# Kernel optimization log

Measured on AMD Instinct MI355X. Metric: run time of the kernel, lower is better.

Reference implementation:

```python
import jax, jax.numpy as jnp
import numpy as np

N = 8192      # nodes
E = 16384     # edges
G = 512       # graphs
IN = 235      # node feature dim (input_dim)
H = 64        # hidden_dim
ED = 52       # edge feature dim


def setup_inputs() -> dict:
    key = jax.random.key(0)
    ks = jax.random.split(key, 24)
    s = lambda fan_in: 1.0 / np.sqrt(fan_in)
    inp = {}
    inp["x"] = jax.random.normal(ks[0], (N, IN), dtype=jnp.float32)
    inp["edge_index"] = jax.random.randint(ks[1], (2, E), 0, N)
    inp["edge_attr"] = jax.random.uniform(ks[2], (E, ED), dtype=jnp.float32)
    inp["batch"] = jnp.sort(jax.random.randint(ks[3], (N,), 0, G))
    # EdgeModel (nn of nnconv1): Linear(52,128) -> Linear(128, 235*64)
    inp["W1"] = jax.random.normal(ks[4], (128, ED), dtype=jnp.float32) * s(ED)
    inp["b1"] = jnp.zeros((128,), jnp.float32)
    inp["W2"] = jax.random.normal(ks[5], (IN * H, 128), dtype=jnp.float32) * s(128)
    inp["b2"] = jnp.zeros((IN * H,), jnp.float32)
    # NNConv root weight and bias
    inp["root"] = jax.random.normal(ks[6], (IN, H), dtype=jnp.float32) * s(IN)
    inp["conv_b"] = jnp.zeros((H,), jnp.float32)
    # MLP head
    inp["fw1"] = jax.random.normal(ks[7], (128, H), dtype=jnp.float32) * s(H)
    inp["fb1"] = jnp.zeros((128,), jnp.float32)
    inp["fw2"] = jax.random.normal(ks[8], (256, 128), dtype=jnp.float32) * s(128)
    inp["fb2"] = jnp.zeros((256,), jnp.float32)
    inp["fw3"] = jax.random.normal(ks[9], (128, 256), dtype=jnp.float32) * s(256)
    inp["fb3"] = jnp.zeros((128,), jnp.float32)
    inp["fw4"] = jax.random.normal(ks[10], (1, 128), dtype=jnp.float32) * s(128)
    inp["fb4"] = jnp.zeros((1,), jnp.float32)
    return inp


def reference(x, edge_index, edge_attr, batch, W1, b1, W2, b2, root, conv_b,
              fw1, fb1, fw2, fb2, fw3, fb3, fw4, fb4):
    src, dst = edge_index[0], edge_index[1]
    # edge MLP -> per-edge weight matrices [E, IN, H]
    h = edge_attr @ W1.T + b1
    w = (h @ W2.T + b2).reshape(E, IN, H)
    # gather source node feats, per-edge matmul, scatter-add to destinations
    msg = jnp.einsum('ei,eih->eh', x[src], w)          # [E, H]
    agg = jax.ops.segment_sum(msg, dst, num_segments=N)  # [N, H]
    out = jax.nn.relu(agg + x @ root + conv_b)           # NNConv + ReLU
    # global mean pool per graph
    summ = jax.ops.segment_sum(out, batch, num_segments=G)
    cnt = jax.ops.segment_sum(jnp.ones((N, 1), out.dtype), batch, num_segments=G)
    pooled = summ / jnp.maximum(cnt, 1.0)                # [G, H]
    # dense MLP head
    y = jax.nn.relu(pooled @ fw1.T + fb1)
    y = jax.nn.relu(y @ fw2.T + fb2)
    y = jax.nn.relu(y @ fw3.T + fb3)
    return y @ fw4.T + fb4                               # [G, 1]
```

## Files before the change

### kernel.cpp

```cpp
#include <hip/hip_runtime.h>
#include <hip/hip_bf16.h>
#include <stdint.h>

#define N_NODES 8192
#define N_EDGES 16384
#define N_GRAPHS 512
#define IN_DIM 235
#define H_DIM 64
#define ED_DIM 52
#define HID1 128
#define KP 256
#define NB 3328
#define NBE 3456
#define NBP 3584

typedef __bf16 bf16x8 __attribute__((ext_vector_type(8)));
typedef float f32x4 __attribute__((ext_vector_type(4)));

static __device__ inline unsigned short f2bf(float f) {
    union { float f; unsigned u; } v; v.f = f;
    unsigned r = v.u + 0x7FFFu + ((v.u >> 16) & 1u);
    return (unsigned short)(r >> 16);
}
static __device__ inline float bf2f(unsigned short s) {
    union { unsigned u; float f; } v; v.u = ((unsigned)s) << 16;
    return v.f;
}

__global__ __launch_bounds__(256) void k_build_bt(const float* __restrict__ W1,
                                                  const float* __restrict__ W2,
                                                  unsigned short* __restrict__ Bt) {
    __shared__ float w1s[13 * HID1];
    __shared__ float w2s[64 * 132];
    const int i = blockIdx.x;
    const int by = blockIdx.y;
    const int t = threadIdx.x;
    const int dbase = by * 13;
    for (int j = t; j < 13 * HID1; j += 256) {
        const int dd = j >> 7, k = j & 127;
        w1s[j] = W1[k * ED_DIM + dbase + dd];
    }
    const float* w2src = W2 + (size_t)i * 64 * HID1;
    for (int j = t; j < 64 * HID1; j += 256) w2s[(j >> 7) * 132 + (j & 127)] = w2src[j];
    __syncthreads();
    const int pend = by * 832 + 832;
    for (int p = by * 832 + t; p < pend; p += 256) {
        const int dd = (p >> 6) - dbase, h = p & 63;
        const float4* w1v = (const float4*)&w1s[dd * HID1];
        const float4* w2v = (const float4*)&w2s[h * 132];
        float acc = 0.f;
        #pragma unroll
        for (int k4 = 0; k4 < HID1 / 4; ++k4) {
            const float4 a = w1v[k4], b = w2v[k4];
            acc += a.x * b.x + a.y * b.y + a.z * b.z + a.w * b.w;
        }
        Bt[(size_t)p * KP + i] = f2bf(acc);
    }
}

__global__ __launch_bounds__(256) void k_build_ext(const float* __restrict__ root,
                                                   const float* __restrict__ W2,
                                                   const float* __restrict__ b1,
                                                   const float* __restrict__ b2,
                                                   unsigned short* __restrict__ Bt) {
    const int j = blockIdx.x;
    const int i = threadIdx.x;
    if (i >= IN_DIM) return;
    float v;
    if (j < 64) {
        v = root[i * H_DIM + j];
    } else {
        const int jj = i * H_DIM + (j - 64);
        float acc = b2[jj];
        const float* w = W2 + (size_t)jj * HID1;
        #pragma unroll 8
        for (int k = 0; k < HID1; ++k) acc += w[k] * b1[k];
        v = acc;
    }
    Bt[(size_t)(NB + j) * KP + i] = f2bf(v);
}

__global__ __launch_bounds__(256) void k_build_a(const float* __restrict__ x,
                                                 unsigned short* __restrict__ A) {
    const int j = blockIdx.x * 256 + threadIdx.x;
    const int n = j >> 8, i = j & 255;
    A[j] = (i < IN_DIM) ? f2bf(x[n * IN_DIM + i]) : (unsigned short)0;
}

__global__ __launch_bounds__(512, 2) void k_gemm(const unsigned short* __restrict__ A,
                                                 const unsigned short* __restrict__ Bt,
                                                 unsigned short* __restrict__ P,
                                                 float* __restrict__ agg,
                                                 float* __restrict__ xb2,
                                                 const float* __restrict__ conv_b) {
    __shared__ unsigned short As[2 * 256 * 32];
    __shared__ unsigned short Bs[2 * 256 * 32];
    const int t = threadIdx.x;
    const int m0 = blockIdx.y * 256, n0 = blockIdx.x * 256;
    const int wid = t >> 6, lane = t & 63;
    const int wm = wid & 1;
    const int wn = wid >> 1;
    const int q = lane >> 4, r16 = lane & 15;

    f32x4 acc[8][4] = {};

    auto stage = [&](int k0, int buf) {
        #pragma unroll
        for (int r = 0; r < 2; ++r) {
            const int idx = r * 512 + t;
            const int row = idx >> 2;
            const int lgrp = ((idx & 3) ^ ((row >> 1) & 3)) * 8;
            const unsigned short* ga = &A[(size_t)(m0 + row) * KP + k0 + lgrp];
            const unsigned short* gb = &Bt[(size_t)(n0 + row) * KP + k0 + lgrp];
            char* la = (char*)As + buf * 16384 + r * 8192 + wid * 1024;
            char* lb = (char*)Bs + buf * 16384 + r * 8192 + wid * 1024;
            __builtin_amdgcn_global_load_lds(
                (const __attribute__((address_space(1))) unsigned int*)ga,
                (__attribute__((address_space(3))) unsigned int*)la, 16, 0, 0);
            __builtin_amdgcn_global_load_lds(
                (const __attribute__((address_space(1))) unsigned int*)gb,
                (__attribute__((address_space(3))) unsigned int*)lb, 16, 0, 0);
        }
    };

    stage(0, 0);
    const int pcq = (q ^ ((r16 >> 1) & 3)) * 8;
    #pragma unroll
    for (int it = 0; it < 8; ++it) {
        __syncthreads();
        if (it < 7) stage((it + 1) * 32, (it + 1) & 1);
        const int bo = (it & 1) * 8192;
        bf16x8 af[8], bfr[4];
        #pragma unroll
        for (int mi = 0; mi < 8; ++mi)
            af[mi] = *(const bf16x8*)(&As[bo + (wm * 128 + mi * 16 + r16) * 32 + pcq]);
        #pragma unroll
        for (int ni = 0; ni < 4; ++ni)
            bfr[ni] = *(const bf16x8*)(&Bs[bo + (wn * 64 + ni * 16 + r16) * 32 + pcq]);
        #pragma unroll
        for (int mi = 0; mi < 8; ++mi)
            #pragma unroll
            for (int ni = 0; ni < 4; ++ni)
                acc[mi][ni] = __builtin_amdgcn_mfma_f32_16x16x32_bf16(
                    bfr[ni], af[mi], acc[mi][ni], 0, 0, 0);
    }

    if (n0 < NB) {
        #pragma unroll
        for (int mi = 0; mi < 8; ++mi)
            #pragma unroll
            for (int ni = 0; ni < 4; ++ni) {
                const int row = m0 + wm * 128 + mi * 16 + r16;
                const int col = n0 + wn * 64 + ni * 16 + q * 4;
                union { unsigned short us[4]; uint2 u2; } pk;
                #pragma unroll
                for (int rr = 0; rr < 4; ++rr) pk.us[rr] = f2bf(acc[mi][ni][rr]);
                *(uint2*)(&P[(size_t)row * NB + col]) = pk.u2;
            }
    } else if (wn < 2) {
        #pragma unroll
        for (int mi = 0; mi < 8; ++mi)
            #pragma unroll
            for (int ni = 0; ni < 4; ++ni) {
                const int row = m0 + wm * 128 + mi * 16 + r16;
                const int cl = ni * 16 + q * 4;
                if (wn == 0) {
                    const float4 cb = *(const float4*)&conv_b[cl];
                    float4 v;
                    v.x = acc[mi][ni][0] + cb.x; v.y = acc[mi][ni][1] + cb.y;
                    v.z = acc[mi][ni][2] + cb.z; v.w = acc[mi][ni][3] + cb.w;
                    *(float4*)(&agg[row * H_DIM + cl]) = v;
                } else {
                    float4 v;
                    v.x = acc[mi][ni][0]; v.y = acc[mi][ni][1];
                    v.z = acc[mi][ni][2]; v.w = acc[mi][ni][3];
                    *(float4*)(&xb2[row * H_DIM + cl]) = v;
                }
            }
    }
}

__global__ __launch_bounds__(256) void k_edge(const int* __restrict__ ei,
                                              const float* __restrict__ ea,
                                              const unsigned short* __restrict__ P,
                                              const float* __restrict__ xb2,
                                              float* __restrict__ agg) {
    const int e = (blockIdx.x * 256 + threadIdx.x) >> 6;
    const int h = threadIdx.x & 63;
    if (e >= N_EDGES) return;
    const int s = ei[e], dst = ei[N_EDGES + e];
    const unsigned short* Pr = P + (size_t)s * NB + h;
    const float* ear = ea + (size_t)e * ED_DIM;

    float eav[ED_DIM];
    #pragma unroll
    for (int d4 = 0; d4 < ED_DIM / 4; ++d4)
        *(float4*)&eav[d4 * 4] = *(const float4*)&ear[d4 * 4];

    unsigned short pv[ED_DIM];
    #pragma unroll
    for (int d = 0; d < ED_DIM; ++d) pv[d] = Pr[d * H_DIM];

    float acc = xb2[s * H_DIM + h];
    #pragma unroll
    for (int d = 0; d < ED_DIM; ++d) acc += eav[d] * bf2f(pv[d]);
    atomicAdd(&agg[dst * H_DIM + h], acc);
}

__global__ __launch_bounds__(256) void k_pool(const float* __restrict__ agg,
                                              const int* __restrict__ batch,
                                              float* __restrict__ psum,
                                              float* __restrict__ pcnt) {
    const int n = (blockIdx.x * 256 + threadIdx.x) >> 6;
    const int h = threadIdx.x & 63;
    if (n >= N_NODES) return;
    const float v = fmaxf(agg[n * H_DIM + h], 0.f);
    const int g = batch[n];
    atomicAdd(&psum[g * H_DIM + h], v);
    if (h == 0) atomicAdd(&pcnt[g], 1.0f);
}

__global__ __launch_bounds__(256) void k_head(const float* __restrict__ psum,
                                              const float* __restrict__ pcnt,
                                              const float* __restrict__ fw1, const float* __restrict__ fb1,
                                              const float* __restrict__ fw2, const float* __restrict__ fb2,
                                              const float* __restrict__ fw3, const float* __restrict__ fb3,
                                              const float* __restrict__ fw4, const float* __restrict__ fb4,
                                              float* __restrict__ out) {
    __shared__ float sp[64], s1[128], s2[256], s3[128];
    const int g = blockIdx.x, t = threadIdx.x;
    if (t < 64) sp[t] = psum[g * 64 + t] / fmaxf(pcnt[g], 1.0f);
    __syncthreads();
    if (t < 128) {
        float a = fb1[t];
        const float* w = fw1 + t * 64;
        #pragma unroll 8
        for (int k = 0; k < 64; ++k) a += sp[k] * w[k];
        s1[t] = fmaxf(a, 0.f);
    }
    __syncthreads();
    {
        float a = fb2[t];
        const float* w = fw2 + t * 128;
        #pragma unroll 8
        for (int k = 0; k < 128; ++k) a += s1[k] * w[k];
        s2[t] = fmaxf(a, 0.f);
    }
    __syncthreads();
    if (t < 128) {
        float a = fb3[t];
        const float* w = fw3 + t * 256;
        #pragma unroll 8
        for (int k = 0; k < 256; ++k) a += s2[k] * w[k];
        s3[t] = fmaxf(a, 0.f);
    }
    __syncthreads();
    if (t < 64) {
        float p = s3[t] * fw4[t] + s3[t + 64] * fw4[t + 64];
        #pragma unroll
        for (int off = 32; off > 0; off >>= 1) p += __shfl_down(p, off);
        if (t == 0) out[g] = p + fb4[0];
    }
}

extern "C" void kernel_launch(void* const* d_in, const int* in_sizes, int n_in,
                              void* d_out, int out_size, void* d_ws, size_t ws_size,
                              hipStream_t stream) {
    const float* x      = (const float*)d_in[0];
    const int*   ei     = (const int*)d_in[1];
    const float* ea     = (const float*)d_in[2];
    const int*   batch  = (const int*)d_in[3];
    const float* W1     = (const float*)d_in[4];
    const float* b1     = (const float*)d_in[5];
    const float* W2     = (const float*)d_in[6];
    const float* b2     = (const float*)d_in[7];
    const float* root   = (const float*)d_in[8];
    const float* conv_b = (const float*)d_in[9];
    const float* fw1 = (const float*)d_in[10]; const float* fb1 = (const float*)d_in[11];
    const float* fw2 = (const float*)d_in[12]; const float* fb2 = (const float*)d_in[13];
    const float* fw3 = (const float*)d_in[14]; const float* fb3 = (const float*)d_in[15];
    const float* fw4 = (const float*)d_in[16]; const float* fb4 = (const float*)d_in[17];
    float* out = (float*)d_out;

    char* ws = (char*)d_ws;
    unsigned short* A   = (unsigned short*)(ws);
    unsigned short* Bt  = (unsigned short*)(ws + 4194304);
    unsigned short* P   = (unsigned short*)(ws + 6029312);
    float* agg  = (float*)(ws + 60555264);
    float* xb2  = (float*)(ws + 62652416);
    float* psum = (float*)(ws + 64749568);
    float* pcnt = (float*)(ws + 64880640);

    hipMemsetAsync(Bt, 0, (size_t)NBP * KP * sizeof(unsigned short), stream);
    hipMemsetAsync(psum, 0, (size_t)(N_GRAPHS * H_DIM + N_GRAPHS) * sizeof(float), stream);

    k_build_bt<<<dim3(IN_DIM, 4), dim3(256), 0, stream>>>(W1, W2, Bt);
    k_build_ext<<<dim3(128), dim3(256), 0, stream>>>(root, W2, b1, b2, Bt);
    k_build_a<<<dim3(N_NODES), dim3(256), 0, stream>>>(x, A);
    k_gemm<<<dim3(NBP / 256, N_NODES / 256), dim3(512), 0, stream>>>(A, Bt, P, agg, xb2, conv_b);
    k_edge<<<dim3(N_EDGES / 4), dim3(256), 0, stream>>>(ei, ea, P, xb2, agg);
    k_pool<<<dim3(N_NODES / 4), dim3(256), 0, stream>>>(agg, batch, psum, pcnt);
    k_head<<<dim3(N_GRAPHS), dim3(256), 0, stream>>>(psum, pcnt, fw1, fb1, fw2, fb2, fw3, fb3, fw4, fb4, out);
}
```

Baseline: 218.1 us.

## Transpose P column layout to h-major and remap GEMM tiles across XCDs

The B matrix columns are reordered so each hidden unit's 52 edge-feature coefficients sit contiguously in P. The edge kernel can then load them as vectorized uint2 reads instead of 52 strided scalar loads, and unpack bf16 pairs with bit ops. The GEMM grid is flattened to 448 blocks and remapped so blocks sharing an M tile land on the same XCD, aiming for better L2 reuse. The risk is that each edge thread now reads a distinct contiguous chunk, so lanes in a wavefront access strided addresses, which may hurt coalescing.

```diff
diff --git a/kernel.cpp b/kernel.cpp
--- a/kernel.cpp
+++ b/kernel.cpp
@@ -22,38 +22,33 @@
     unsigned r = v.u + 0x7FFFu + ((v.u >> 16) & 1u);
     return (unsigned short)(r >> 16);
 }
-static __device__ inline float bf2f(unsigned short s) {
-    union { unsigned u; float f; } v; v.u = ((unsigned)s) << 16;
-    return v.f;
-}
 
 __global__ __launch_bounds__(256) void k_build_bt(const float* __restrict__ W1,
                                                   const float* __restrict__ W2,
                                                   unsigned short* __restrict__ Bt) {
-    __shared__ float w1s[13 * HID1];
-    __shared__ float w2s[64 * 132];
+    __shared__ float w1s[ED_DIM * HID1];
+    __shared__ float w2s[16 * 132];
     const int i = blockIdx.x;
     const int by = blockIdx.y;
     const int t = threadIdx.x;
-    const int dbase = by * 13;
-    for (int j = t; j < 13 * HID1; j += 256) {
-        const int dd = j >> 7, k = j & 127;
-        w1s[j] = W1[k * ED_DIM + dbase + dd];
-    }
-    const float* w2src = W2 + (size_t)i * 64 * HID1;
-    for (int j = t; j < 64 * HID1; j += 256) w2s[(j >> 7) * 132 + (j & 127)] = w2src[j];
-    __syncthreads();
-    const int pend = by * 832 + 832;
-    for (int p = by * 832 + t; p < pend; p += 256) {
-        const int dd = (p >> 6) - dbase, h = p & 63;
-        const float4* w1v = (const float4*)&w1s[dd * HID1];
-        const float4* w2v = (const float4*)&w2s[h * 132];
+    for (int j = t; j < ED_DIM * HID1; j += 256) {
+        const int d = j >> 7, k = j & 127;
+        w1s[j] = W1[k * ED_DIM + d];
+    }
+    const float* w2src = W2 + ((size_t)i * 64 + by * 16) * HID1;
+    for (int j = t; j < 16 * HID1; j += 256) w2s[(j >> 7) * 132 + (j & 127)] = w2src[j];
+    __syncthreads();
+    for (int pl = t; pl < 832; pl += 256) {
+        const int hh = pl / 52, d = pl - hh * 52;
+        const float4* w1v = (const float4*)&w1s[d * HID1];
+        const float4* w2v = (const float4*)&w2s[hh * 132];
         float acc = 0.f;
         #pragma unroll
         for (int k4 = 0; k4 < HID1 / 4; ++k4) {
             const float4 a = w1v[k4], b = w2v[k4];
             acc += a.x * b.x + a.y * b.y + a.z * b.z + a.w * b.w;
         }
+        const int p = by * 832 + pl;
         Bt[(size_t)p * KP + i] = f2bf(acc);
     }
 }
@@ -96,7 +91,11 @@
     __shared__ unsigned short As[2 * 256 * 32];
     __shared__ unsigned short Bs[2 * 256 * 32];
     const int t = threadIdx.x;
-    const int m0 = blockIdx.y * 256, n0 = blockIdx.x * 256;
+    const int lin = blockIdx.x;
+    const int xcd = lin & 7, bi = lin >> 3;
+    const int mt = (bi / 14) * 8 + xcd;
+    const int nt = bi % 14;
+    const int m0 = mt * 256, n0 = nt * 256;
     const int wid = t >> 6, lane = t & 63;
     const int wm = wid & 1;
     const int wn = wid >> 1;
@@ -189,21 +188,25 @@
     const int h = threadIdx.x & 63;
     if (e >= N_EDGES) return;
     const int s = ei[e], dst = ei[N_EDGES + e];
-    const unsigned short* Pr = P + (size_t)s * NB + h;
-    const float* ear = ea + (size_t)e * ED_DIM;
-
-    float eav[ED_DIM];
+    const uint2* Pr = (const uint2*)(P + (size_t)s * NB + h * ED_DIM);
+    const float4* ev = (const float4*)(ea + (size_t)e * ED_DIM);
+
+    uint2 pv[13];
     #pragma unroll
-    for (int d4 = 0; d4 < ED_DIM / 4; ++d4)
-        *(float4*)&eav[d4 * 4] = *(const float4*)&ear[d4 * 4];
-
-    unsigned short pv[ED_DIM];
+    for (int j = 0; j < 13; ++j) pv[j] = Pr[j];
+    float4 eav[13];
     #pragma unroll
-    for (int d = 0; d < ED_DIM; ++d) pv[d] = Pr[d * H_DIM];
+    for (int j = 0; j < 13; ++j) eav[j] = ev[j];
 
     float acc = xb2[s * H_DIM + h];
     #pragma unroll
-    for (int d = 0; d < ED_DIM; ++d) acc += eav[d] * bf2f(pv[d]);
+    for (int j = 0; j < 13; ++j) {
+        union { unsigned u; float f; } a0, a1, b0, b1;
+        a0.u = pv[j].x << 16; a1.u = pv[j].x & 0xffff0000u;
+        b0.u = pv[j].y << 16; b1.u = pv[j].y & 0xffff0000u;
+        acc += eav[j].x * a0.f + eav[j].y * a1.f
+             + eav[j].z * b0.f + eav[j].w * b1.f;
+    }
     atomicAdd(&agg[dst * H_DIM + h], acc);
 }
 
@@ -297,7 +300,7 @@
     k_build_bt<<<dim3(IN_DIM, 4), dim3(256), 0, stream>>>(W1, W2, Bt);
     k_build_ext<<<dim3(128), dim3(256), 0, stream>>>(root, W2, b1, b2, Bt);
     k_build_a<<<dim3(N_NODES), dim3(256), 0, stream>>>(x, A);
-    k_gemm<<<dim3(NBP / 256, N_NODES / 256), dim3(512), 0, stream>>>(A, Bt, P, agg, xb2, conv_b);
+    k_gemm<<<dim3(448), dim3(512), 0, stream>>>(A, Bt, P, agg, xb2, conv_b);
     k_edge<<<dim3(N_EDGES / 4), dim3(256), 0, stream>>>(ei, ea, P, xb2, agg);
     k_pool<<<dim3(N_NODES / 4), dim3(256), 0, stream>>>(agg, batch, psum, pcnt);
     k_head<<<dim3(N_GRAPHS), dim3(256), 0, stream>>>(psum, pcnt, fw1, fb1, fw2, fb2, fw3, fb3, fw4, fb4, out);
```

Measured after the change: 247.6 us. 1.14x slower.
